# Kernel optimization log

Measured on AMD Instinct MI355X. Metric: run time of the kernel, lower is better.

## Reference

```python
import jax, jax.numpy as jnp
import numpy as np

IN_FEATURES = 512
OUT_FEATURES = 512
B_EXP = 2.0
EPS = 1e-12  # torch F.normalize eps


def setup_inputs() -> dict:
    key = jax.random.key(0)
    kz, kw = jax.random.split(key)
    z = jax.random.normal(kz, (100000, IN_FEATURES), dtype=jnp.float32)
    weight = jax.random.normal(kw, (OUT_FEATURES, IN_FEATURES), dtype=jnp.float32) * (1.0 / np.sqrt(IN_FEATURES))
    return {"z": z, "weight": weight}


def reference(z, weight):
    # lin = z @ W^T : [N, out]
    lin = jnp.einsum('ni,oi->no', z, weight)
    # row-wise L2 normalize (torch F.normalize: x / max(||x||, eps))
    z_norm = z / jnp.maximum(jnp.linalg.norm(z, axis=1, keepdims=True), EPS)
    w_norm = weight / jnp.maximum(jnp.linalg.norm(weight, axis=1, keepdims=True), EPS)
    cos = jnp.einsum('ni,oi->no', z_norm, w_norm)
    scale = jnp.abs(cos) ** (B_EXP - 1.0)
    return lin * scale
```

## Files before the change

### kernel.cpp

```cpp
#include <hip/hip_runtime.h>
#include <hip/hip_bf16.h>
#include <stdint.h>


constexpr int KDIM = 512;
constexpr int NDIM = 512;

typedef __attribute__((ext_vector_type(8))) short bf16x8;
typedef __attribute__((ext_vector_type(4))) float f32x4;

__device__ __forceinline__ uint32_t pk_bf16(float a, float b) {
  __hip_bfloat162 h = __float22bfloat162_rn(make_float2(a, b));
  union { __hip_bfloat162 h2; uint32_t u; } c;
  c.h2 = h;
  return c.u;
}

__device__ __forceinline__ void gload_lds16(const void* g, void* lds) {
  __builtin_amdgcn_global_load_lds(
      (const __attribute__((address_space(1))) uint32_t*)(uintptr_t)g,
      (__attribute__((address_space(3))) uint32_t*)(uintptr_t)lds,
      16, 0, 0);
}

__global__ __launch_bounds__(128) void prep_w(const float* __restrict__ w,
                                              unsigned short* __restrict__ wbt,
                                              float* __restrict__ cninv) {
  const int row = blockIdx.x;
  const int t   = threadIdx.x;
  const int k0  = t * 4;
  f32x4 v = *(const f32x4*)(w + (size_t)row * KDIM + k0);
  float s = v.x * v.x + v.y * v.y + v.z * v.z + v.w * v.w;

  uint2 p;
  p.x = pk_bf16(v.x, v.y);
  p.y = pk_bf16(v.z, v.w);
  const int c  = k0 >> 5;
  const int k8 = (k0 >> 3) & 3;
  *(uint2*)(wbt + ((size_t)c * 2048 + k8 * 512 + row) * 8 + (k0 & 7)) = p;

  #pragma unroll
  for (int off = 32; off > 0; off >>= 1) s += __shfl_down(s, off, 64);
  __shared__ float red[2];
  if ((t & 63) == 0) red[t >> 6] = s;
  __syncthreads();
  if (t == 0) cninv[row] = 1.0f / fmaxf(sqrtf(red[0] + red[1]), 1e-12f);
}

__global__ __launch_bounds__(512, 2) void gemm_bcos(const float* __restrict__ z,
                                                    const unsigned short* __restrict__ wbt,
                                                    const float* __restrict__ cninv,
                                                    float* __restrict__ out, int M) {
  __shared__ unsigned short As[64 * 512];
  __shared__ unsigned short Bs[2][2048 * 8];
  __shared__ float rowsq[64];
  __shared__ float rinv_s[64];

  const int t    = threadIdx.x;
  const int w    = t >> 6;
  const int lane = t & 63;
  const int lrow = lane & 15;
  const int quad = lane >> 4;
  const int mb   = blockIdx.x;
  const int wn   = w * 64;

  #pragma unroll
  for (int i = 0; i < 4; ++i)
    gload_lds16(wbt + (size_t)(t + 512 * i) * 8, &Bs[0][(t + 512 * i) * 8]);
  #pragma unroll
  for (int i = 0; i < 4; ++i)
    gload_lds16(wbt + (size_t)(2048 + t + 512 * i) * 8, &Bs[1][(t + 512 * i) * 8]);

  #pragma unroll
  for (int rr = 0; rr < 8; ++rr) {
    const int rl = w * 8 + rr;
    int rg = mb * 64 + rl;
    if (rg >= M) rg = M - 1;
    const float* zp = z + (size_t)rg * KDIM;
    float s = 0.0f;
    #pragma unroll
    for (int j = 0; j < 2; ++j) {
      f32x4 v = *(const f32x4*)(zp + j * 256 + lane * 4);
      s += v.x * v.x + v.y * v.y + v.z * v.z + v.w * v.w;
      uint2 p;
      p.x = pk_bf16(v.x, v.y);
      p.y = pk_bf16(v.z, v.w);
      const int cb = (j * 512 + lane * 8) ^ (rr << 4);
      *(uint2*)((char*)As + rl * 1024 + cb) = p;
    }
    #pragma unroll
    for (int off = 32; off > 0; off >>= 1) s += __shfl_down(s, off, 64);
    if (lane == 0) rowsq[rl] = s;
  }
  __syncthreads();
  if (t < 64) rinv_s[t] = 1.0f / fmaxf(sqrtf(rowsq[t]), 1e-12f);
  __syncthreads();

  f32x4 acc[4][4];
  #pragma unroll
  for (int i = 0; i < 4; ++i)
    #pragma unroll
    for (int j = 0; j < 4; ++j) acc[i][j] = (f32x4)0.0f;

  const int qs = (quad * 16) ^ ((lrow & 7) << 4);

  bf16x8 a[2][4];
  #pragma unroll
  for (int mt = 0; mt < 4; ++mt)
    a[0][mt] = *(const bf16x8*)((const char*)As + ((mt * 16 + lrow) << 10) + (0 ^ qs));

  #pragma unroll
  for (int c = 0; c < 16; ++c) {
    if (c < 15) asm volatile("s_waitcnt vmcnt(4)" ::: "memory");
    else        asm volatile("s_waitcnt vmcnt(0)" ::: "memory");
    __builtin_amdgcn_s_barrier();
    asm volatile("" ::: "memory");

    bf16x8 b[4];
    #pragma unroll
    for (int nt = 0; nt < 4; ++nt)
      b[nt] = *(const bf16x8*)&Bs[c & 1][(quad * 512 + wn + nt * 16 + lrow) * 8];
    if (c < 15) {
      #pragma unroll
      for (int mt = 0; mt < 4; ++mt)
        a[(c + 1) & 1][mt] = *(const bf16x8*)((const char*)As +
            ((mt * 16 + lrow) << 10) + (((c + 1) * 64) ^ qs));
    }

    __builtin_amdgcn_s_setprio(1);
    #pragma unroll
    for (int mt = 0; mt < 4; ++mt)
      #pragma unroll
      for (int nt = 0; nt < 4; ++nt)
        acc[mt][nt] = __builtin_amdgcn_mfma_f32_16x16x32_bf16(a[c & 1][mt], b[nt], acc[mt][nt], 0, 0, 0);
    __builtin_amdgcn_s_setprio(0);

    asm volatile("" ::: "memory");
    __builtin_amdgcn_s_barrier();
    if (c + 2 < 16) {
      #pragma unroll
      for (int i = 0; i < 4; ++i)
        gload_lds16(wbt + ((size_t)(c + 2) * 2048 + t + 512 * i) * 8,
                    &Bs[c & 1][(t + 512 * i) * 8]);
    }
  }

  #pragma unroll
  for (int nt = 0; nt < 4; ++nt) {
    const int colg = wn + nt * 16 + lrow;
    const float cv = cninv[colg];
    #pragma unroll
    for (int mt = 0; mt < 4; ++mt) {
      const int rl = mt * 16 + quad * 4;
      #pragma unroll
      for (int i = 0; i < 4; ++i) {
        const int rowg = mb * 64 + rl + i;
        if (rowg < M) {
          const float v = acc[mt][nt][i];
          __builtin_nontemporal_store(v * fabsf(v) * rinv_s[rl + i] * cv,
                                      &out[(size_t)rowg * NDIM + colg]);
        }
      }
    }
  }
}

extern "C" void kernel_launch(void* const* d_in, const int* in_sizes, int n_in,
                              void* d_out, int out_size, void* d_ws, size_t ws_size,
                              hipStream_t stream) {
  const float* z = (const float*)d_in[0];
  const float* w = (const float*)d_in[1];
  float* out = (float*)d_out;
  const int M = in_sizes[0] / KDIM;

  unsigned short* wbt = (unsigned short*)d_ws;
  float* cninv = (float*)((char*)d_ws + (size_t)NDIM * KDIM * 2);

  prep_w<<<dim3(NDIM), dim3(128), 0, stream>>>(w, wbt, cninv);

  dim3 grid((M + 63) / 64);
  gemm_bcos<<<grid, dim3(512), 0, stream>>>(z, wbt, cninv, out, M);
}
```

Measured before the change: 422.7 us.

## Split N across two blocks and stream A tiles through a double-buffered pipeline

Each workgroup now computes a 64x256 output tile with 256 threads, where it previously computed 64x512 with 512 threads, so the grid doubles along N. The full 64x512 bf16 A tile in LDS is replaced by small double-buffered 32-wide K slices. Each slice is converted from fp32 in registers one chunk ahead and overlapped with the MFMA work, and row norms accumulate along the way. This cuts LDS use so three blocks fit per CU and removes the upfront serial z-conversion phase. The cost is that every z row is read twice from global memory, once per N half, and there is an extra barrier per K step.

```diff
diff --git a/kernel.cpp b/kernel.cpp
--- a/kernel.cpp
+++ b/kernel.cpp
@@ -8,6 +8,7 @@
 
 typedef __attribute__((ext_vector_type(8))) short bf16x8;
 typedef __attribute__((ext_vector_type(4))) float f32x4;
+typedef __attribute__((ext_vector_type(4))) uint32_t u32x4;
 
 __device__ __forceinline__ uint32_t pk_bf16(float a, float b) {
   __hip_bfloat162 h = __float22bfloat162_rn(make_float2(a, b));
@@ -47,12 +48,12 @@
   if (t == 0) cninv[row] = 1.0f / fmaxf(sqrtf(red[0] + red[1]), 1e-12f);
 }
 
-__global__ __launch_bounds__(512, 2) void gemm_bcos(const float* __restrict__ z,
+__global__ __launch_bounds__(256, 3) void gemm_bcos(const float* __restrict__ z,
                                                     const unsigned short* __restrict__ wbt,
                                                     const float* __restrict__ cninv,
                                                     float* __restrict__ out, int M) {
-  __shared__ unsigned short As[64 * 512];
-  __shared__ unsigned short Bs[2][2048 * 8];
+  __shared__ unsigned short As[2][64 * 40];
+  __shared__ unsigned short Bs[2][1024 * 8];
   __shared__ float rowsq[64];
   __shared__ float rinv_s[64];
 
@@ -61,93 +62,121 @@
   const int lane = t & 63;
   const int lrow = lane & 15;
   const int quad = lane >> 4;
-  const int mb   = blockIdx.x;
+  const int nb   = blockIdx.x;
+  const int mb   = blockIdx.y;
   const int wn   = w * 64;
 
+  const int arow = t >> 2;
+  const int aseg = t & 3;
+  int rg = mb * 64 + arow;
+  if (rg >= M) rg = M - 1;
+  const float* zrow = z + (size_t)rg * KDIM + aseg * 8;
+  char* const adst0 = (char*)As[0] + arow * 80 + aseg * 16;
+  char* const adst1 = (char*)As[1] + arow * 80 + aseg * 16;
+
+  float sq = 0.0f;
+
+  f32x4 a0A = *(const f32x4*)(zrow + 0);
+  f32x4 a1A = *(const f32x4*)(zrow + 4);
+  f32x4 a0B = *(const f32x4*)(zrow + 32);
+  f32x4 a1B = *(const f32x4*)(zrow + 36);
+
+  #pragma unroll
+  for (int i = 0; i < 4; ++i) {
+    const int gl = t + 256 * i;
+    gload_lds16(wbt + ((size_t)(gl >> 8) * 512 + nb * 256 + (gl & 255)) * 8,
+                &Bs[0][gl * 8]);
+  }
+  #pragma unroll
+  for (int i = 0; i < 4; ++i) {
+    const int gl = t + 256 * i;
+    gload_lds16(wbt + ((size_t)2048 + (gl >> 8) * 512 + nb * 256 + (gl & 255)) * 8,
+                &Bs[1][gl * 8]);
+  }
+
+  {
+    sq += a0A.x*a0A.x + a0A.y*a0A.y + a0A.z*a0A.z + a0A.w*a0A.w
+        + a1A.x*a1A.x + a1A.y*a1A.y + a1A.z*a1A.z + a1A.w*a1A.w;
+    u32x4 p;
+    p.x = pk_bf16(a0A.x, a0A.y); p.y = pk_bf16(a0A.z, a0A.w);
+    p.z = pk_bf16(a1A.x, a1A.y); p.w = pk_bf16(a1A.z, a1A.w);
+    *(u32x4*)adst0 = p;
+  }
+
+  f32x4 acc[4][4];
   #pragma unroll
   for (int i = 0; i < 4; ++i)
-    gload_lds16(wbt + (size_t)(t + 512 * i) * 8, &Bs[0][(t + 512 * i) * 8]);
-  #pragma unroll
-  for (int i = 0; i < 4; ++i)
-    gload_lds16(wbt + (size_t)(2048 + t + 512 * i) * 8, &Bs[1][(t + 512 * i) * 8]);
-
-  #pragma unroll
-  for (int rr = 0; rr < 8; ++rr) {
-    const int rl = w * 8 + rr;
-    int rg = mb * 64 + rl;
-    if (rg >= M) rg = M - 1;
-    const float* zp = z + (size_t)rg * KDIM;
-    float s = 0.0f;
-    #pragma unroll
-    for (int j = 0; j < 2; ++j) {
-      f32x4 v = *(const f32x4*)(zp + j * 256 + lane * 4);
-      s += v.x * v.x + v.y * v.y + v.z * v.z + v.w * v.w;
-      uint2 p;
-      p.x = pk_bf16(v.x, v.y);
-      p.y = pk_bf16(v.z, v.w);
-      const int cb = (j * 512 + lane * 8) ^ (rr << 4);
-      *(uint2*)((char*)As + rl * 1024 + cb) = p;
+    #pragma unroll
+    for (int j = 0; j < 4; ++j) acc[i][j] = (f32x4)0.0f;
+
+  asm volatile("s_waitcnt vmcnt(4)" ::: "memory");
+  asm volatile("s_waitcnt lgkmcnt(0)" ::: "memory");
+  __builtin_amdgcn_s_barrier();
+  asm volatile("" ::: "memory");
+
+  #pragma unroll
+  for (int c = 0; c < 16; ++c) {
+    bf16x8 bfr[4], afr[4];
+    #pragma unroll
+    for (int nt = 0; nt < 4; ++nt)
+      bfr[nt] = *(const bf16x8*)&Bs[c & 1][(quad * 256 + wn + nt * 16 + lrow) * 8];
+    #pragma unroll
+    for (int mt = 0; mt < 4; ++mt)
+      afr[mt] = *(const bf16x8*)((const char*)As[c & 1] + (mt * 16 + lrow) * 80 + quad * 16);
+
+    __builtin_amdgcn_s_setprio(1);
+    #pragma unroll
+    for (int mt = 0; mt < 4; ++mt)
+      #pragma unroll
+      for (int nt = 0; nt < 4; ++nt)
+        acc[mt][nt] = __builtin_amdgcn_mfma_f32_16x16x32_bf16(afr[mt], bfr[nt], acc[mt][nt], 0, 0, 0);
+    __builtin_amdgcn_s_setprio(0);
+
+    if (c < 15) {
+      asm volatile("" ::: "memory");
+      __builtin_amdgcn_s_barrier();
+      asm volatile("" ::: "memory");
+
+      if (c + 2 < 16) {
+        f32x4 n0 = *(const f32x4*)(zrow + (c + 2) * 32);
+        f32x4 n1 = *(const f32x4*)(zrow + (c + 2) * 32 + 4);
+        if ((c & 1) == 0) { a0A = n0; a1A = n1; } else { a0B = n0; a1B = n1; }
+        #pragma unroll
+        for (int i = 0; i < 4; ++i) {
+          const int gl = t + 256 * i;
+          gload_lds16(wbt + ((size_t)(c + 2) * 2048 + (gl >> 8) * 512 + nb * 256 + (gl & 255)) * 8,
+                      &Bs[c & 1][gl * 8]);
+        }
+      }
+      {
+        f32x4 v0 = ((c & 1) == 0) ? a0B : a0A;
+        f32x4 v1 = ((c & 1) == 0) ? a1B : a1A;
+        sq += v0.x*v0.x + v0.y*v0.y + v0.z*v0.z + v0.w*v0.w
+            + v1.x*v1.x + v1.y*v1.y + v1.z*v1.z + v1.w*v1.w;
+        u32x4 p;
+        p.x = pk_bf16(v0.x, v0.y); p.y = pk_bf16(v0.z, v0.w);
+        p.z = pk_bf16(v1.x, v1.y); p.w = pk_bf16(v1.z, v1.w);
+        *(u32x4*)(((c & 1) == 0) ? adst1 : adst0) = p;
+      }
+
+      if (c + 2 < 16) asm volatile("s_waitcnt vmcnt(6)" ::: "memory");
+      else            asm volatile("s_waitcnt vmcnt(0)" ::: "memory");
+      asm volatile("s_waitcnt lgkmcnt(0)" ::: "memory");
+      __builtin_amdgcn_s_barrier();
+      asm volatile("" ::: "memory");
     }
-    #pragma unroll
-    for (int off = 32; off > 0; off >>= 1) s += __shfl_down(s, off, 64);
-    if (lane == 0) rowsq[rl] = s;
-  }
+  }
+
+  sq += __shfl_down(sq, 2, 64);
+  sq += __shfl_down(sq, 1, 64);
+  if (aseg == 0) rowsq[arow] = sq;
   __syncthreads();
   if (t < 64) rinv_s[t] = 1.0f / fmaxf(sqrtf(rowsq[t]), 1e-12f);
   __syncthreads();
 
-  f32x4 acc[4][4];
-  #pragma unroll
-  for (int i = 0; i < 4; ++i)
-    #pragma unroll
-    for (int j = 0; j < 4; ++j) acc[i][j] = (f32x4)0.0f;
-
-  const int qs = (quad * 16) ^ ((lrow & 7) << 4);
-
-  bf16x8 a[2][4];
-  #pragma unroll
-  for (int mt = 0; mt < 4; ++mt)
-    a[0][mt] = *(const bf16x8*)((const char*)As + ((mt * 16 + lrow) << 10) + (0 ^ qs));
-
-  #pragma unroll
-  for (int c = 0; c < 16; ++c) {
-    if (c < 15) asm volatile("s_waitcnt vmcnt(4)" ::: "memory");
-    else        asm volatile("s_waitcnt vmcnt(0)" ::: "memory");
-    __builtin_amdgcn_s_barrier();
-    asm volatile("" ::: "memory");
-
-    bf16x8 b[4];
-    #pragma unroll
-    for (int nt = 0; nt < 4; ++nt)
-      b[nt] = *(const bf16x8*)&Bs[c & 1][(quad * 512 + wn + nt * 16 + lrow) * 8];
-    if (c < 15) {
-      #pragma unroll
-      for (int mt = 0; mt < 4; ++mt)
-        a[(c + 1) & 1][mt] = *(const bf16x8*)((const char*)As +
-            ((mt * 16 + lrow) << 10) + (((c + 1) * 64) ^ qs));
-    }
-
-    __builtin_amdgcn_s_setprio(1);
-    #pragma unroll
-    for (int mt = 0; mt < 4; ++mt)
-      #pragma unroll
-      for (int nt = 0; nt < 4; ++nt)
-        acc[mt][nt] = __builtin_amdgcn_mfma_f32_16x16x32_bf16(a[c & 1][mt], b[nt], acc[mt][nt], 0, 0, 0);
-    __builtin_amdgcn_s_setprio(0);
-
-    asm volatile("" ::: "memory");
-    __builtin_amdgcn_s_barrier();
-    if (c + 2 < 16) {
-      #pragma unroll
-      for (int i = 0; i < 4; ++i)
-        gload_lds16(wbt + ((size_t)(c + 2) * 2048 + t + 512 * i) * 8,
-                    &Bs[c & 1][(t + 512 * i) * 8]);
-    }
-  }
-
   #pragma unroll
   for (int nt = 0; nt < 4; ++nt) {
-    const int colg = wn + nt * 16 + lrow;
+    const int colg = nb * 256 + wn + nt * 16 + lrow;
     const float cv = cninv[colg];
     #pragma unroll
     for (int mt = 0; mt < 4; ++mt) {
@@ -178,6 +207,6 @@
 
   prep_w<<<dim3(NDIM), dim3(128), 0, stream>>>(w, wbt, cninv);
 
-  dim3 grid((M + 63) / 64);
-  gemm_bcos<<<grid, dim3(512), 0, stream>>>(z, wbt, cninv, out, M);
-}
+  dim3 grid(2, (M + 63) / 64);
+  gemm_bcos<<<grid, dim3(256), 0, stream>>>(z, wbt, cninv, out, M);
+}
```

After: 430.8 us. Within noise of the previous version (+1.9%).
